# Kernel optimization log

Measured on AMD Instinct MI355X. Metric: run time of the kernel, lower is better.

The kernel has to match this reference:

```python
import jax, jax.numpy as jnp
import numpy as np

B, T, C, H = 2, 2048, 1024, 16
HD = C // H  # head dim = 64


def setup_inputs() -> dict:
    key = jax.random.key(0)
    ks = jax.random.split(key, 5)
    s = 0.02  # GPT-style init scale for weights
    return {
        "x": jax.random.normal(ks[0], (B, T, C), dtype=jnp.float32),
        "Wq": jax.random.normal(ks[1], (C, C), dtype=jnp.float32) * s,
        "bq": jnp.zeros((C,), dtype=jnp.float32),
        "Wk": jax.random.normal(ks[2], (C, C), dtype=jnp.float32) * s,
        "bk": jnp.zeros((C,), dtype=jnp.float32),
        "Wv": jax.random.normal(ks[3], (C, C), dtype=jnp.float32) * s,
        "bv": jnp.zeros((C,), dtype=jnp.float32),
        "Wp": jax.random.normal(ks[4], (C, C), dtype=jnp.float32) * s,
        "bp": jnp.zeros((C,), dtype=jnp.float32),
    }


def reference(x, Wq, bq, Wk, bk, Wv, bv, Wp, bp):
    b, t, c = x.shape
    # torch nn.Linear: y = x @ W.T + b  (W is [out, in])
    def heads(W, bias):
        y = jnp.einsum("btc,oc->bto", x, W) + bias
        return y.reshape(b, t, H, HD).transpose(0, 2, 1, 3)  # [B,H,T,hd]

    q = heads(Wq, bq)
    k = heads(Wk, bk)
    v = heads(Wv, bv)

    scale = 1.0 / np.sqrt(HD).astype(np.float32)
    att = jnp.einsum("bhqd,bhkd->bhqk", q, k) * scale  # [B,H,T,T]
    causal = jnp.tril(jnp.ones((t, t), dtype=bool))
    att = jnp.where(causal[None, None], att, -jnp.inf)
    att = jax.nn.softmax(att, axis=-1)
    # attn_pdrop = 0.0 -> dropout is identity
    y = jnp.einsum("bhqk,bhkd->bhqd", att, v)  # [B,H,T,hd]
    y = y.transpose(0, 2, 1, 3).reshape(b, t, c)
    y = jnp.einsum("btc,oc->bto", y, Wp) + bp  # resid_pdrop = 0.0
    return y
```

## Files before the change

kernel.cpp:

```cpp
#include <hip/hip_runtime.h>
#include <hip/hip_bf16.h>

using bf16 = __hip_bfloat16;
typedef __attribute__((ext_vector_type(8))) short short8;
typedef __attribute__((ext_vector_type(4))) float floatx4;

#define B_  2
#define T_  2048
#define C_  1024
#define H_  16
#define HD_ 64
#define BT_ (B_*T_)
#define NX_ ((size_t)BT_*C_)
#define NW_ ((size_t)C_*C_)
#define PSTR2 40
#define KSCQ 0.1803368801f

__device__ __forceinline__ void gl2lds16(const bf16* g, bf16* l) {
    __builtin_amdgcn_global_load_lds((const __attribute__((address_space(1))) unsigned int*)g,
                                     (__attribute__((address_space(3))) unsigned int*)l,
                                     16, 0, 0);
}

__global__ __launch_bounds__(256) void cvt_f32_bf16(
    const float* __restrict__ x,
    const float* __restrict__ Wq, const float* __restrict__ Wk,
    const float* __restrict__ Wv, const float* __restrict__ Wp,
    bf16* __restrict__ xb, bf16* __restrict__ wqb, bf16* __restrict__ wkb,
    bf16* __restrict__ wvb, bf16* __restrict__ wpb)
{
    size_t i4 = ((size_t)blockIdx.x * 256 + threadIdx.x) * 4;
    const float* src; bf16* dst; size_t off;
    if (i4 < NX_) { src = x; dst = xb; off = i4; }
    else {
        size_t j = i4 - NX_;
        int r = (int)(j >> 20);
        off = j & (NW_ - 1);
        src = (r==0) ? Wq : (r==1) ? Wk : (r==2) ? Wv : Wp;
        dst = (r==0) ? wqb : (r==1) ? wkb : (r==2) ? wvb : wpb;
    }
    float4 v = *(const float4*)(src + off);
    union { bf16 h[4]; uint2 u; } o;
    o.h[0] = __float2bfloat16(v.x); o.h[1] = __float2bfloat16(v.y);
    o.h[2] = __float2bfloat16(v.z); o.h[3] = __float2bfloat16(v.w);
    *(uint2*)(dst + off) = o.u;
}

__global__ __launch_bounds__(256) void qkv_gemm(
    const bf16* __restrict__ x,
    const bf16* __restrict__ Wq, const float* __restrict__ bq,
    const bf16* __restrict__ Wk, const float* __restrict__ bk,
    const bf16* __restrict__ Wv, const float* __restrict__ bv,
    bf16* __restrict__ qo, bf16* __restrict__ ko, bf16* __restrict__ vt)
{
    __shared__ __align__(16) bf16 As[128*32];
    __shared__ __align__(16) bf16 Bs[128*32];

    const int tid  = threadIdx.x;
    const int w    = tid >> 6, lane = tid & 63;
    const int g    = lane >> 4, c16 = lane & 15;
    const int wr   = w >> 1,    wc  = w & 1;
    const int mtile = blockIdx.x, ntile = blockIdx.y;
    const int wsel  = ntile >> 3;
    const bf16*  W    = (wsel==0) ? Wq : (wsel==1 ? Wk : Wv);
    const float* bias = (wsel==0) ? bq : (wsel==1 ? bk : bv);
    const float oscale = (wsel==0) ? KSCQ : 1.0f;
    const int nbase  = (ntile & 7) * 128;

    const bf16* ag = x + (size_t)(mtile*128)*C_;
    const bf16* bg = W + (size_t)nbase*C_;

    floatx4 acc[4][4] = {};

    for (int k0 = 0; k0 < C_; k0 += 32) {
        #pragma unroll
        for (int p = 0; p < 2; ++p) {
            int cb = p*256 + w*64;
            int c  = cb + lane;
            gl2lds16(ag + (size_t)(c>>2)*C_ + k0 + (c&3)*8, As + cb*8);
            gl2lds16(bg + (size_t)(c>>2)*C_ + k0 + (c&3)*8, Bs + cb*8);
        }
        __syncthreads();

        short8 af[4], bfr[4];
        #pragma unroll
        for (int i = 0; i < 4; ++i)
            af[i] = *(const short8*)(As + (wr*64 + i*16 + c16)*32 + g*8);
        #pragma unroll
        for (int j = 0; j < 4; ++j)
            bfr[j] = *(const short8*)(Bs + (wc*64 + j*16 + c16)*32 + g*8);
        #pragma unroll
        for (int i = 0; i < 4; ++i)
            #pragma unroll
            for (int j = 0; j < 4; ++j)
                acc[i][j] = __builtin_amdgcn_mfma_f32_16x16x32_bf16(af[i], bfr[j], acc[i][j], 0, 0, 0);
        __syncthreads();
    }

    #pragma unroll
    for (int i = 0; i < 4; ++i) {
        int m0 = mtile*128 + wr*64 + i*16 + g*4;
        #pragma unroll
        for (int j = 0; j < 4; ++j) {
            int n = nbase + wc*64 + j*16 + c16;
            float bvf = bias[n];
            if (wsel == 2) {
                int bb = m0 >> 11, t0 = m0 & (T_-1);
                int hh = n >> 6,  hd = n & 63;
                union { bf16 hv[4]; uint2 u; } tmp;
                #pragma unroll
                for (int r = 0; r < 4; ++r) tmp.hv[r] = __float2bfloat16(acc[i][j][r] + bvf);
                *(uint2*)(vt + ((size_t)((bb*H_ + hh)*64 + hd))*T_ + t0) = tmp.u;
            } else {
                bf16* dst = (wsel==0) ? qo : ko;
                #pragma unroll
                for (int r = 0; r < 4; ++r)
                    dst[(size_t)(m0+r)*C_ + n] = __float2bfloat16((acc[i][j][r] + bvf) * oscale);
            }
        }
    }
}

__global__ __launch_bounds__(256, 4) void attn(
    const bf16* __restrict__ q, const bf16* __restrict__ k,
    const bf16* __restrict__ vt, bf16* __restrict__ y)
{
    __shared__ __align__(16) bf16 Ks[16*512];
    __shared__ __align__(16) bf16 Vs[16*512];
    __shared__ __align__(16) bf16 Ps[4][16*PSTR2];

    const int tid = threadIdx.x, w = tid >> 6, lane = tid & 63;
    const int g = lane >> 4, c16 = lane & 15;
    const int beta = blockIdx.x;
    const int qraw = beta & 31, rhi = beta >> 5;
    const int h = rhi & 15, b = rhi >> 4;
    const int qt = (h & 8) ? 31 - qraw : qraw;
    const int qbase = qt*64 + w*16;
    const int nit = (qt + 2) >> 1;
    const int qglob = qbase + c16;

    const bf16* kbase = k  + ((size_t)(b*T_))*C_ + h*64;
    const bf16* vbase = vt + ((size_t)(b*H_ + h))*64*T_;

    short8 aq[2];
    #pragma unroll
    for (int kg = 0; kg < 2; ++kg)
        aq[kg] = *(const short8*)(q + ((size_t)(b*T_ + qglob))*C_ + h*64 + kg*32 + g*8);

    const short ONEB = 0x3F80;
    const short8 ones = {ONEB,ONEB,ONEB,ONEB,ONEB,ONEB,ONEB,ONEB};

    floatx4 accO[4] = {};
    floatx4 lacc = {};

    for (int kt = 0; kt < nit; ++kt) {
        #pragma unroll
        for (int p = 0; p < 4; ++p) {
            int f = w*4 + p;
            int ctk = f >> 1, kg = f & 1;
            gl2lds16(kbase + (size_t)(kt*128 + ctk*16 + c16)*C_ + kg*32 + g*8, Ks + f*512);
            gl2lds16(vbase + (size_t)(p*16 + c16)*T_ + kt*128 + w*32 + g*8,    Vs + f*512);
        }
        __syncthreads();

        floatx4 s[8];
        #pragma unroll
        for (int ct = 0; ct < 8; ++ct) {
            floatx4 a = {0.f, 0.f, 0.f, 0.f};
            #pragma unroll
            for (int kg = 0; kg < 2; ++kg) {
                short8 kb = *(const short8*)(Ks + (ct*2 + kg)*512 + lane*8);
                a = __builtin_amdgcn_mfma_f32_16x16x32_bf16(kb, aq[kg], a, 0, 0, 0);
            }
            s[ct] = a;
        }

        if (kt == nit-1) {
            #pragma unroll
            for (int ct = 0; ct < 8; ++ct)
                #pragma unroll
                for (int r = 0; r < 4; ++r) {
                    int key = kt*128 + ct*16 + g*4 + r;
                    if (key > qglob) s[ct][r] = -1e30f;
                }
        }

        #pragma unroll
        for (int ks = 0; ks < 4; ++ks) {
            #pragma unroll
            for (int half = 0; half < 2; ++half) {
                int ct = ks*2 + half;
                float p0 = exp2f(s[ct][0]);
                float p1 = exp2f(s[ct][1]);
                float p2 = exp2f(s[ct][2]);
                float p3 = exp2f(s[ct][3]);
                union { __hip_bfloat162 h2[2]; uint2 u; } pk;
                pk.h2[0] = __float22bfloat162_rn(float2{p0, p1});
                pk.h2[1] = __float22bfloat162_rn(float2{p2, p3});
                *(uint2*)(Ps[w] + c16*PSTR2 + half*16 + g*4) = pk.u;
            }
            short8 pa = *(const short8*)(Ps[w] + c16*PSTR2 + g*8);
            lacc = __builtin_amdgcn_mfma_f32_16x16x32_bf16(pa, ones, lacc, 0, 0, 0);
            #pragma unroll
            for (int nt = 0; nt < 4; ++nt) {
                short8 vb = *(const short8*)(Vs + (ks*4 + nt)*512 + lane*8);
                accO[nt] = __builtin_amdgcn_mfma_f32_16x16x32_bf16(pa, vb, accO[nt], 0, 0, 0);
            }
        }
        __syncthreads();
    }

    float ir[4];
    #pragma unroll
    for (int r = 0; r < 4; ++r) ir[r] = __builtin_amdgcn_rcpf(lacc[r]);
    #pragma unroll
    for (int nt = 0; nt < 4; ++nt)
        #pragma unroll
        for (int r = 0; r < 4; ++r) {
            int row = qbase + g*4 + r;
            float o = accO[nt][r] * ir[r];
            y[((size_t)(b*T_ + row))*C_ + h*64 + nt*16 + c16] = __float2bfloat16(o);
        }
}

__global__ __launch_bounds__(256) void proj_gemm(
    const bf16* __restrict__ yin, const bf16* __restrict__ Wp, const float* __restrict__ bp,
    float* __restrict__ out)
{
    __shared__ __align__(16) bf16 As[128*32];
    __shared__ __align__(16) bf16 Bs[128*32];

    const int tid = threadIdx.x;
    const int w = tid >> 6, lane = tid & 63;
    const int g = lane >> 4, c16 = lane & 15;
    const int wr = w >> 1, wc = w & 1;
    const int mtile = blockIdx.x, ntile = blockIdx.y;
    const int nbase = ntile * 128;

    const bf16* ag = yin + (size_t)(mtile*128)*C_;
    const bf16* bg = Wp  + (size_t)nbase*C_;

    floatx4 acc[4][4] = {};

    for (int k0 = 0; k0 < C_; k0 += 32) {
        #pragma unroll
        for (int p = 0; p < 2; ++p) {
            int cb = p*256 + w*64;
            int c  = cb + lane;
            gl2lds16(ag + (size_t)(c>>2)*C_ + k0 + (c&3)*8, As + cb*8);
            gl2lds16(bg + (size_t)(c>>2)*C_ + k0 + (c&3)*8, Bs + cb*8);
        }
        __syncthreads();

        short8 af[4], bfr[4];
        #pragma unroll
        for (int i = 0; i < 4; ++i)
            af[i] = *(const short8*)(As + (wr*64 + i*16 + c16)*32 + g*8);
        #pragma unroll
        for (int j = 0; j < 4; ++j)
            bfr[j] = *(const short8*)(Bs + (wc*64 + j*16 + c16)*32 + g*8);
        #pragma unroll
        for (int i = 0; i < 4; ++i)
            #pragma unroll
            for (int j = 0; j < 4; ++j)
                acc[i][j] = __builtin_amdgcn_mfma_f32_16x16x32_bf16(af[i], bfr[j], acc[i][j], 0, 0, 0);
        __syncthreads();
    }

    #pragma unroll
    for (int i = 0; i < 4; ++i) {
        int m0 = mtile*128 + wr*64 + i*16 + g*4;
        #pragma unroll
        for (int j = 0; j < 4; ++j) {
            int n = nbase + wc*64 + j*16 + c16;
            float bvf = bp[n];
            #pragma unroll
            for (int r = 0; r < 4; ++r)
                out[(size_t)(m0+r)*C_ + n] = acc[i][j][r] + bvf;
        }
    }
}

extern "C" void kernel_launch(void* const* d_in, const int* in_sizes, int n_in,
                              void* d_out, int out_size, void* d_ws, size_t ws_size,
                              hipStream_t stream) {
    const float* x  = (const float*)d_in[0];
    const float* Wq = (const float*)d_in[1];
    const float* bq = (const float*)d_in[2];
    const float* Wk = (const float*)d_in[3];
    const float* bk = (const float*)d_in[4];
    const float* Wv = (const float*)d_in[5];
    const float* bv = (const float*)d_in[6];
    const float* Wp = (const float*)d_in[7];
    const float* bp = (const float*)d_in[8];

    bf16* xb  = (bf16*)d_ws;
    bf16* wqb = xb  + NX_;
    bf16* wkb = wqb + NW_;
    bf16* wvb = wkb + NW_;
    bf16* wpb = wvb + NW_;
    bf16* qw  = wpb + NW_;
    bf16* kw  = qw  + NX_;
    bf16* vt  = kw  + NX_;
    bf16* yw  = vt  + NX_;

    const int cvt_blocks = (int)((NX_ + 4*NW_) / (4*256));
    cvt_f32_bf16<<<cvt_blocks, 256, 0, stream>>>(x, Wq, Wk, Wv, Wp, xb, wqb, wkb, wvb, wpb);
    qkv_gemm<<<dim3(32, 24), 256, 0, stream>>>(xb, wqb, bq, wkb, bk, wvb, bv, qw, kw, vt);
    attn    <<<1024, 256, 0, stream>>>(qw, kw, vt, yw);
    proj_gemm<<<dim3(32, 8), 256, 0, stream>>>(yw, wpb, bp, (float*)d_out);
}
```

Measured before the change: 195.2 us.

## Load K and V tiles directly from global into registers in attention

Removes the shared-memory staging of K and V tiles, along with both block-wide barriers per iteration, in the attention kernel. Each wave now reads its MFMA operands straight from global memory (relying on L1/L2 caching, since all four waves read the same K/V data). This cuts LDS traffic and synchronisation and frees shared memory for occupancy, but multiplies global/cache load requests by four and exposes load latency without explicit prefetch.

```diff
diff --git a/kernel.cpp b/kernel.cpp
--- a/kernel.cpp
+++ b/kernel.cpp
@@ -125,8 +125,6 @@
     const bf16* __restrict__ q, const bf16* __restrict__ k,
     const bf16* __restrict__ vt, bf16* __restrict__ y)
 {
-    __shared__ __align__(16) bf16 Ks[16*512];
-    __shared__ __align__(16) bf16 Vs[16*512];
     __shared__ __align__(16) bf16 Ps[4][16*PSTR2];
 
     const int tid = threadIdx.x, w = tid >> 6, lane = tid & 63;
@@ -139,8 +137,8 @@
     const int nit = (qt + 2) >> 1;
     const int qglob = qbase + c16;
 
-    const bf16* kbase = k  + ((size_t)(b*T_))*C_ + h*64;
-    const bf16* vbase = vt + ((size_t)(b*H_ + h))*64*T_;
+    const bf16* kp = k  + ((size_t)(b*T_) + c16)*C_ + h*64 + g*8;
+    const bf16* vp = vt + (((size_t)(b*H_ + h))*64 + c16)*T_ + g*8;
 
     short8 aq[2];
     #pragma unroll
@@ -154,24 +152,17 @@
     floatx4 lacc = {};
 
     for (int kt = 0; kt < nit; ++kt) {
-        #pragma unroll
-        for (int p = 0; p < 4; ++p) {
-            int f = w*4 + p;
-            int ctk = f >> 1, kg = f & 1;
-            gl2lds16(kbase + (size_t)(kt*128 + ctk*16 + c16)*C_ + kg*32 + g*8, Ks + f*512);
-            gl2lds16(vbase + (size_t)(p*16 + c16)*T_ + kt*128 + w*32 + g*8,    Vs + f*512);
-        }
-        __syncthreads();
+        const bf16* kpt = kp + (size_t)(kt*128)*C_;
+        const bf16* vpt = vp + kt*128;
 
         floatx4 s[8];
         #pragma unroll
         for (int ct = 0; ct < 8; ++ct) {
+            short8 kb0 = *(const short8*)(kpt + (size_t)(ct*16)*C_);
+            short8 kb1 = *(const short8*)(kpt + (size_t)(ct*16)*C_ + 32);
             floatx4 a = {0.f, 0.f, 0.f, 0.f};
-            #pragma unroll
-            for (int kg = 0; kg < 2; ++kg) {
-                short8 kb = *(const short8*)(Ks + (ct*2 + kg)*512 + lane*8);
-                a = __builtin_amdgcn_mfma_f32_16x16x32_bf16(kb, aq[kg], a, 0, 0, 0);
-            }
+            a = __builtin_amdgcn_mfma_f32_16x16x32_bf16(kb0, aq[0], a, 0, 0, 0);
+            a = __builtin_amdgcn_mfma_f32_16x16x32_bf16(kb1, aq[1], a, 0, 0, 0);
             s[ct] = a;
         }
 
@@ -187,6 +178,10 @@
 
         #pragma unroll
         for (int ks = 0; ks < 4; ++ks) {
+            short8 vb[4];
+            #pragma unroll
+            for (int nt = 0; nt < 4; ++nt)
+                vb[nt] = *(const short8*)(vpt + (size_t)(nt*16)*T_ + ks*32);
             #pragma unroll
             for (int half = 0; half < 2; ++half) {
                 int ct = ks*2 + half;
@@ -202,12 +197,9 @@
             short8 pa = *(const short8*)(Ps[w] + c16*PSTR2 + g*8);
             lacc = __builtin_amdgcn_mfma_f32_16x16x32_bf16(pa, ones, lacc, 0, 0, 0);
             #pragma unroll
-            for (int nt = 0; nt < 4; ++nt) {
-                short8 vb = *(const short8*)(Vs + (ks*4 + nt)*512 + lane*8);
-                accO[nt] = __builtin_amdgcn_mfma_f32_16x16x32_bf16(pa, vb, accO[nt], 0, 0, 0);
-            }
-        }
-        __syncthreads();
+            for (int nt = 0; nt < 4; ++nt)
+                accO[nt] = __builtin_amdgcn_mfma_f32_16x16x32_bf16(pa, vb[nt], accO[nt], 0, 0, 0);
+        }
     }
 
     float ir[4];
```

Result: slower. 271.6 us (+39.2%).

## Enlarge attention query tile to 128 rows per block for K/V reuse

Applied to the files above, without the earlier changes.

The attention kernel now has each wave handle 32 query rows (two 16-row halves) instead of 16, so a block covers 128 queries and the grid shrinks from 1024 to 512 blocks. Each K/V tile loaded into LDS is reused by twice as many MFMAs, halving global K/V traffic and barriers per query. Score computation, masking and exp are fused into a single pass that writes P straight to a wider LDS buffer. The trade-off is more registers (launch bounds lowered to 2 blocks), fewer blocks to fill the device, and coarser causal load balancing, handled by mirroring tiles across the batch index.

```diff
diff --git a/kernel.cpp b/kernel.cpp
--- a/kernel.cpp
+++ b/kernel.cpp
@@ -13,7 +13,7 @@
 #define BT_ (B_*T_)
 #define NX_ ((size_t)BT_*C_)
 #define NW_ ((size_t)C_*C_)
-#define PSTR2 40
+#define PSTR 136
 #define KSCQ 0.1803368801f
 
 __device__ __forceinline__ void gl2lds16(const bf16* g, bf16* l) {
@@ -121,37 +121,39 @@
     }
 }
 
-__global__ __launch_bounds__(256, 4) void attn(
+__global__ __launch_bounds__(256, 2) void attn(
     const bf16* __restrict__ q, const bf16* __restrict__ k,
     const bf16* __restrict__ vt, bf16* __restrict__ y)
 {
     __shared__ __align__(16) bf16 Ks[16*512];
     __shared__ __align__(16) bf16 Vs[16*512];
-    __shared__ __align__(16) bf16 Ps[4][16*PSTR2];
+    __shared__ __align__(16) bf16 Ps[4][32*PSTR];
 
     const int tid = threadIdx.x, w = tid >> 6, lane = tid & 63;
     const int g = lane >> 4, c16 = lane & 15;
     const int beta = blockIdx.x;
-    const int qraw = beta & 31, rhi = beta >> 5;
-    const int h = rhi & 15, b = rhi >> 4;
-    const int qt = (h & 8) ? 31 - qraw : qraw;
-    const int qbase = qt*64 + w*16;
-    const int nit = (qt + 2) >> 1;
-    const int qglob = qbase + c16;
+    const int qraw = beta & 15;
+    const int h = (beta >> 4) & 15;
+    const int b = beta >> 8;
+    const int qt = b ? 15 - qraw : qraw;
+    const int nit = qt + 1;
+    const int qwave = qt*128 + w*32;
 
     const bf16* kbase = k  + ((size_t)(b*T_))*C_ + h*64;
     const bf16* vbase = vt + ((size_t)(b*H_ + h))*64*T_;
 
-    short8 aq[2];
+    short8 aq[2][2];
     #pragma unroll
-    for (int kg = 0; kg < 2; ++kg)
-        aq[kg] = *(const short8*)(q + ((size_t)(b*T_ + qglob))*C_ + h*64 + kg*32 + g*8);
+    for (int qh = 0; qh < 2; ++qh)
+        #pragma unroll
+        for (int kg = 0; kg < 2; ++kg)
+            aq[kg][qh] = *(const short8*)(q + ((size_t)(b*T_ + qwave + qh*16 + c16))*C_ + h*64 + kg*32 + g*8);
 
     const short ONEB = 0x3F80;
     const short8 ones = {ONEB,ONEB,ONEB,ONEB,ONEB,ONEB,ONEB,ONEB};
 
-    floatx4 accO[4] = {};
-    floatx4 lacc = {};
+    floatx4 accO[4][2] = {};
+    floatx4 lacc[2] = {};
 
     for (int kt = 0; kt < nit; ++kt) {
         #pragma unroll
@@ -163,64 +165,62 @@
         }
         __syncthreads();
 
-        floatx4 s[8];
+        const bool lastt = (kt == nit-1);
+
         #pragma unroll
         for (int ct = 0; ct < 8; ++ct) {
-            floatx4 a = {0.f, 0.f, 0.f, 0.f};
-            #pragma unroll
-            for (int kg = 0; kg < 2; ++kg) {
-                short8 kb = *(const short8*)(Ks + (ct*2 + kg)*512 + lane*8);
-                a = __builtin_amdgcn_mfma_f32_16x16x32_bf16(kb, aq[kg], a, 0, 0, 0);
+            short8 kb0 = *(const short8*)(Ks + (ct*2+0)*512 + lane*8);
+            short8 kb1 = *(const short8*)(Ks + (ct*2+1)*512 + lane*8);
+            #pragma unroll
+            for (int qh = 0; qh < 2; ++qh) {
+                floatx4 a = {0.f, 0.f, 0.f, 0.f};
+                a = __builtin_amdgcn_mfma_f32_16x16x32_bf16(kb0, aq[0][qh], a, 0, 0, 0);
+                a = __builtin_amdgcn_mfma_f32_16x16x32_bf16(kb1, aq[1][qh], a, 0, 0, 0);
+                if (lastt) {
+                    int qg = qwave + qh*16 + c16;
+                    #pragma unroll
+                    for (int r = 0; r < 4; ++r) {
+                        int key = kt*128 + ct*16 + g*4 + r;
+                        if (key > qg) a[r] = -1e30f;
+                    }
+                }
+                union { __hip_bfloat162 h2[2]; uint2 u; } pk;
+                pk.h2[0] = __float22bfloat162_rn(float2{exp2f(a[0]), exp2f(a[1])});
+                pk.h2[1] = __float22bfloat162_rn(float2{exp2f(a[2]), exp2f(a[3])});
+                *(uint2*)(Ps[w] + (qh*16 + c16)*PSTR + ct*16 + g*4) = pk.u;
             }
-            s[ct] = a;
-        }
-
-        if (kt == nit-1) {
-            #pragma unroll
-            for (int ct = 0; ct < 8; ++ct)
-                #pragma unroll
-                for (int r = 0; r < 4; ++r) {
-                    int key = kt*128 + ct*16 + g*4 + r;
-                    if (key > qglob) s[ct][r] = -1e30f;
-                }
         }
 
         #pragma unroll
         for (int ks = 0; ks < 4; ++ks) {
-            #pragma unroll
-            for (int half = 0; half < 2; ++half) {
-                int ct = ks*2 + half;
-                float p0 = exp2f(s[ct][0]);
-                float p1 = exp2f(s[ct][1]);
-                float p2 = exp2f(s[ct][2]);
-                float p3 = exp2f(s[ct][3]);
-                union { __hip_bfloat162 h2[2]; uint2 u; } pk;
-                pk.h2[0] = __float22bfloat162_rn(float2{p0, p1});
-                pk.h2[1] = __float22bfloat162_rn(float2{p2, p3});
-                *(uint2*)(Ps[w] + c16*PSTR2 + half*16 + g*4) = pk.u;
-            }
-            short8 pa = *(const short8*)(Ps[w] + c16*PSTR2 + g*8);
-            lacc = __builtin_amdgcn_mfma_f32_16x16x32_bf16(pa, ones, lacc, 0, 0, 0);
+            short8 pa0 = *(const short8*)(Ps[w] + (c16     )*PSTR + ks*32 + g*8);
+            short8 pa1 = *(const short8*)(Ps[w] + (16 + c16)*PSTR + ks*32 + g*8);
+            lacc[0] = __builtin_amdgcn_mfma_f32_16x16x32_bf16(pa0, ones, lacc[0], 0, 0, 0);
+            lacc[1] = __builtin_amdgcn_mfma_f32_16x16x32_bf16(pa1, ones, lacc[1], 0, 0, 0);
             #pragma unroll
             for (int nt = 0; nt < 4; ++nt) {
                 short8 vb = *(const short8*)(Vs + (ks*4 + nt)*512 + lane*8);
-                accO[nt] = __builtin_amdgcn_mfma_f32_16x16x32_bf16(pa, vb, accO[nt], 0, 0, 0);
+                accO[nt][0] = __builtin_amdgcn_mfma_f32_16x16x32_bf16(pa0, vb, accO[nt][0], 0, 0, 0);
+                accO[nt][1] = __builtin_amdgcn_mfma_f32_16x16x32_bf16(pa1, vb, accO[nt][1], 0, 0, 0);
             }
         }
         __syncthreads();
     }
 
-    float ir[4];
     #pragma unroll
-    for (int r = 0; r < 4; ++r) ir[r] = __builtin_amdgcn_rcpf(lacc[r]);
-    #pragma unroll
-    for (int nt = 0; nt < 4; ++nt)
-        #pragma unroll
-        for (int r = 0; r < 4; ++r) {
-            int row = qbase + g*4 + r;
-            float o = accO[nt][r] * ir[r];
-            y[((size_t)(b*T_ + row))*C_ + h*64 + nt*16 + c16] = __float2bfloat16(o);
-        }
+    for (int qh = 0; qh < 2; ++qh) {
+        float ir[4];
+        #pragma unroll
+        for (int r = 0; r < 4; ++r) ir[r] = __builtin_amdgcn_rcpf(lacc[qh][r]);
+        #pragma unroll
+        for (int nt = 0; nt < 4; ++nt)
+            #pragma unroll
+            for (int r = 0; r < 4; ++r) {
+                int row = qwave + qh*16 + g*4 + r;
+                float o = accO[nt][qh][r] * ir[r];
+                y[((size_t)(b*T_ + row))*C_ + h*64 + nt*16 + c16] = __float2bfloat16(o);
+            }
+    }
 }
 
 __global__ __launch_bounds__(256) void proj_gemm(
@@ -307,6 +307,6 @@
     const int cvt_blocks = (int)((NX_ + 4*NW_) / (4*256));
     cvt_f32_bf16<<<cvt_blocks, 256, 0, stream>>>(x, Wq, Wk, Wv, Wp, xb, wqb, wkb, wvb, wpb);
     qkv_gemm<<<dim3(32, 24), 256, 0, stream>>>(xb, wqb, bq, wkb, bk, wvb, bv, qw, kw, vt);
-    attn    <<<1024, 256, 0, stream>>>(qw, kw, vt, yw);
+    attn    <<<512, 256, 0, stream>>>(qw, kw, vt, yw);
     proj_gemm<<<dim3(32, 8), 256, 0, stream>>>(yw, wpb, bp, (float*)d_out);
 }
```

After: 207.5 us. 6.3% more time.
